# Performance work log

Hardware: AMD Instinct MI355X
Metric: run time of the kernel (lower is better)

## Reference

```python
import jax, jax.numpy as jnp
import numpy as np

BIAS = 1.0
SIGMA = 0.5
EPS = 1e-5


def mrf_loss(gen, target):
    # gen, target: [B, C, H, W]
    mean_t = jnp.mean(target, axis=1, keepdims=True)
    gf = gen - mean_t
    tf = target - mean_t
    gn = gf / jnp.linalg.norm(gf, axis=1, keepdims=True)
    tn = tf / jnp.linalg.norm(tf, axis=1, keepdims=True)
    B, C, H, W = target.shape
    # 1x1 patches of target, ordered by spatial position (matches unfold h,w order)
    patches = tn.transpose(0, 2, 3, 1).reshape(B, H * W, C)  # [B, P, C]
    # per-sample conv2d with 1x1 kernels == batched GEMM
    sim = jnp.einsum('bpc,bchw->bphw', patches, gn)  # [B, P, H, W]
    cosine_dist = -(sim - 1.0) / 2.0
    relative = cosine_dist / (jnp.min(cosine_dist, axis=1, keepdims=True) + EPS)
    dist = jnp.exp((BIAS - relative) / SIGMA)
    cs = dist / jnp.sum(dist, axis=1, keepdims=True)
    k_max = jnp.max(cs.reshape(B, H * W, -1), axis=2)  # [B, P]
    div_mrf = jnp.mean(k_max, axis=1)  # [B]
    return jnp.sum(-jnp.log(div_mrf))


def setup_inputs() -> dict:
    key = jax.random.key(0)
    k1, k2, k3, k4 = jax.random.split(key, 4)
    return {
        'gen_relu3_2': jax.random.normal(k1, (4, 256, 64, 64), dtype=jnp.float32),
        'tar_relu3_2': jax.random.normal(k2, (4, 256, 64, 64), dtype=jnp.float32),
        'gen_relu4_2': jax.random.normal(k3, (4, 512, 32, 32), dtype=jnp.float32),
        'tar_relu4_2': jax.random.normal(k4, (4, 512, 32, 32), dtype=jnp.float32),
    }


def reference(gen_relu3_2, tar_relu3_2, gen_relu4_2, tar_relu4_2):
    # style layers: relu3_2 (w=1.0), relu4_2 (w=1.0); content layers: relu4_2 (w=1.0)
    m3 = mrf_loss(gen_relu3_2, tar_relu3_2)
    m4 = mrf_loss(gen_relu4_2, tar_relu4_2)
    style_loss = (1.0 * m3 + 1.0 * m4) * 1.0  # l_s = 1.0
    content_loss = (1.0 * m4) * 1.0           # l_c = 1.0
    return style_loss + content_loss
```

## Files before the change

### kernel.cpp

```cpp
#include <hip/hip_runtime.h>
#include <math.h>


#define MRF_EPS 1e-5f
#define LOG2E 1.44269504088896340736f

typedef __attribute__((ext_vector_type(8))) short bf16x8;
typedef __attribute__((ext_vector_type(4))) float f32x4;
typedef unsigned short ushort_t;
struct __align__(8) ushort4_t { ushort_t x, y, z, w; };
struct __align__(16) ushort8_t { ushort_t v[8]; };

__device__ __forceinline__ ushort_t f2bf(float x) {
    unsigned u = __float_as_uint(x);
    u += 0x7FFFu + ((u >> 16) & 1u);
    return (ushort_t)(u >> 16);
}
__device__ __forceinline__ float bf2f(ushort_t u) {
    return __uint_as_float(((unsigned)u) << 16);
}

typedef __attribute__((address_space(1))) const unsigned int gu32;
typedef __attribute__((address_space(3))) unsigned int lu32;
__device__ __forceinline__ void gload16(const ushort_t* g, ushort_t* l) {
    __builtin_amdgcn_global_load_lds((gu32*)(uintptr_t)g, (lu32*)(uintptr_t)l,
                                     16, 0, 0);
}

template <int C>
__device__ __forceinline__ void prep_body(
    const float* __restrict__ gen, const float* __restrict__ tar,
    ushort_t* __restrict__ gnT, ushort_t* __restrict__ tnT,
    int S, int b, int bx, char* __restrict__ smem) {
    constexpr int KN = C / 64;
    constexpr int KC = C / 8;
    constexpr int CP = C + 8;
    const int tid = threadIdx.x, pq = tid & 3, cs = tid >> 2;
    const int s0 = bx * 16;

    f32x4* red  = (f32x4*)smem;
    f32x4* red2 = (f32x4*)(smem + 16384);
    ushort_t* tileG = (ushort_t*)smem;
    ushort_t* tileT = tileG + 16 * CP;
    float* sm  = (float*)(smem + 33280);
    float* srt = sm + 16;
    float* srg = sm + 32;

    const float* g = gen + (size_t)b * C * S + s0 + pq * 4;
    const float* t = tar + (size_t)b * C * S + s0 + pq * 4;

    f32x4 gv[KN], tv[KN];
    f32x4 st = {0.f, 0.f, 0.f, 0.f}, st2 = st, sg = st, sg2 = st;
#pragma unroll
    for (int k = 0; k < KN; k++) {
        tv[k] = *(const f32x4*)(t + (size_t)(cs + 64 * k) * S);
        gv[k] = *(const f32x4*)(g + (size_t)(cs + 64 * k) * S);
        st += tv[k]; st2 += tv[k] * tv[k]; sg += gv[k]; sg2 += gv[k] * gv[k];
    }
    red[(0 * 4 + pq) * 64 + cs] = st;  red[(1 * 4 + pq) * 64 + cs] = st2;
    red[(2 * 4 + pq) * 64 + cs] = sg;  red[(3 * 4 + pq) * 64 + cs] = sg2;
    __syncthreads();
    if (tid < 64) {
        int s_ = tid >> 4, p_ = (tid >> 2) & 3, part = tid & 3;
        f32x4 s = red[(s_ * 4 + p_) * 64 + part * 16];
#pragma unroll
        for (int j = 1; j < 16; j++) s += red[(s_ * 4 + p_) * 64 + part * 16 + j];
        red2[(s_ * 4 + p_) * 4 + part] = s;
    }
    __syncthreads();
    if (tid < 4) {
        f32x4 sts  = red2[(0*4+tid)*4+0] + red2[(0*4+tid)*4+1] + red2[(0*4+tid)*4+2] + red2[(0*4+tid)*4+3];
        f32x4 st2s = red2[(1*4+tid)*4+0] + red2[(1*4+tid)*4+1] + red2[(1*4+tid)*4+2] + red2[(1*4+tid)*4+3];
        f32x4 sgs  = red2[(2*4+tid)*4+0] + red2[(2*4+tid)*4+1] + red2[(2*4+tid)*4+2] + red2[(2*4+tid)*4+3];
        f32x4 sg2s = red2[(3*4+tid)*4+0] + red2[(3*4+tid)*4+1] + red2[(3*4+tid)*4+2] + red2[(3*4+tid)*4+3];
        f32x4 m, vrt, vrg;
        float invC = 1.f / (float)C;
#pragma unroll
        for (int e = 0; e < 4; e++) {
            float mm = sts[e] * invC;
            m[e] = mm;
            vrt[e] = rsqrtf(st2s[e] - mm * sts[e]);
            vrg[e] = rsqrtf(sg2s[e] - 2.f * mm * sgs[e] + mm * sts[e]);
        }
        *(f32x4*)&sm[tid * 4] = m;
        *(f32x4*)&srt[tid * 4] = vrt;
        *(f32x4*)&srg[tid * 4] = vrg;
    }
    __syncthreads();
    f32x4 m4  = *(f32x4*)&sm[pq * 4];
    f32x4 rt4 = *(f32x4*)&srt[pq * 4];
    f32x4 rg4 = *(f32x4*)&srg[pq * 4];
#pragma unroll
    for (int k = 0; k < KN; k++) {
        int c = cs + 64 * k;
#pragma unroll
        for (int e = 0; e < 4; e++) {
            tileG[(pq * 4 + e) * CP + c] = f2bf((gv[k][e] - m4[e]) * rg4[e]);
            tileT[(pq * 4 + e) * CP + c] = f2bf((tv[k][e] - m4[e]) * rt4[e]);
        }
    }
    __syncthreads();
    const int lm = tid & 15;
    const int r16 = s0 >> 4;
    size_t obase = (size_t)b * (size_t)S * C;
#pragma unroll
    for (int j = 0; j < KC / 16; j++) {
        int ch = (tid >> 4) + 16 * j;
        size_t off = obase + (((size_t)r16 * KC + ch) * 16 + lm) * 8;
        *(ushort8_t*)(gnT + off) = *(const ushort8_t*)&tileG[lm * CP + ch * 8];
        *(ushort8_t*)(tnT + off) = *(const ushort8_t*)&tileT[lm * CP + ch * 8];
    }
}

__global__ __launch_bounds__(256) void prep_all(
    const float* __restrict__ gen3, const float* __restrict__ tar3,
    const float* __restrict__ gen4, const float* __restrict__ tar4,
    ushort_t* __restrict__ gnT3, ushort_t* __restrict__ tnT3,
    ushort_t* __restrict__ gnT4, ushort_t* __restrict__ tnT4) {
    __shared__ __align__(16) char smem[33536];
    int bid = blockIdx.x;
    if (bid < 256) {
        int z = bid >> 6, bx = bid & 63;
        prep_body<512>(gen4, tar4, gnT4, tnT4, 1024, z, bx, smem);
    } else {
        bid -= 256;
        int z = bid >> 8, bx = bid & 255;
        prep_body<256>(gen3, tar3, gnT3, tnT3, 4096, z, bx, smem);
    }
}

template <int K>
__device__ __forceinline__ void gemm_body(
    const ushort_t* __restrict__ A, const ushort_t* __restrict__ B,
    ushort_t* __restrict__ sim, float* __restrict__ cmPart,
    int S, int bx, int by, ushort_t* __restrict__ lds) {
    const int tid = threadIdx.x;
    const int lane = tid & 63, wave = tid >> 6;
    const int wm = (wave & 1) * 64, wn = (wave >> 1) * 64;
    const int lm = lane & 15, quad = lane >> 4;
    const int q0 = bx * 128;

    constexpr int KC = K / 8;
    constexpr int KB = K / 32;

    const ushort_t* segsrc[4];
    ushort_t* segdst[4];
#pragma unroll
    for (int i = 0; i < 4; i++) {
        int s = wave * 4 + i;
        segsrc[i] = (s < 8)
            ? A + ((size_t)(by * 8 + s) * KC) * 128 + lane * 8
            : B + ((size_t)(bx * 8 + (s - 8)) * KC) * 128 + lane * 8;
        segdst[i] = lds + s * 512;
    }

    auto stage = [&](int buf, int kb) {
#pragma unroll
        for (int i = 0; i < 4; i++)
            gload16(segsrc[i] + (size_t)kb * 512, segdst[i] + buf * 8192);
    };

    f32x4 acc[4][4];
#pragma unroll
    for (int t = 0; t < 4; t++)
#pragma unroll
        for (int u = 0; u < 4; u++) acc[t][u] = (f32x4){0.f, 0.f, 0.f, 0.f};

    stage(0, 0);
    stage(1, 1);
    asm volatile("s_waitcnt vmcnt(4)" ::: "memory");
    __builtin_amdgcn_s_barrier();
    __builtin_amdgcn_sched_barrier(0);

    const ushort_t* lA = lds + (wm >> 4) * 512 + quad * 128 + lm * 8;
    const ushort_t* lB = lds + 4096 + (wn >> 4) * 512 + quad * 128 + lm * 8;

#pragma unroll
    for (int kb = 0; kb < KB; kb++) {
        const int cur = (kb % 3) * 8192;
        if (kb + 2 < KB) stage((kb + 2) % 3, kb + 2);
        bf16x8 a[4], b[4];
#pragma unroll
        for (int t = 0; t < 4; t++) {
            a[t] = *(const bf16x8*)(lA + cur + t * 512);
            b[t] = *(const bf16x8*)(lB + cur + t * 512);
        }
        __builtin_amdgcn_s_setprio(1);
#pragma unroll
        for (int t = 0; t < 4; t++)
#pragma unroll
            for (int u = 0; u < 4; u++)
                acc[t][u] = __builtin_amdgcn_mfma_f32_16x16x32_bf16(a[t], b[u], acc[t][u], 0, 0, 0);
        __builtin_amdgcn_s_setprio(0);
        if (kb + 1 < KB) {
            if (kb + 2 < KB) asm volatile("s_waitcnt vmcnt(4)" ::: "memory");
            else             asm volatile("s_waitcnt vmcnt(0)" ::: "memory");
            __builtin_amdgcn_s_barrier();
            __builtin_amdgcn_sched_barrier(0);
        }
    }

    int nQB = S >> 7;
    size_t base = ((size_t)(by * nQB + bx)) * 16384
                + (size_t)(wave * 4096 + quad * 128 + lm * 8);
    float cmax[4] = {-INFINITY, -INFINITY, -INFINITY, -INFINITY};
#pragma unroll
    for (int t2 = 0; t2 < 2; t2++)
#pragma unroll
        for (int u = 0; u < 4; u++) {
            f32x4 v0 = acc[t2 * 2][u], v1 = acc[t2 * 2 + 1][u];
            ushort8_t o;
            o.v[0] = f2bf(v0.x); o.v[1] = f2bf(v0.y); o.v[2] = f2bf(v0.z); o.v[3] = f2bf(v0.w);
            o.v[4] = f2bf(v1.x); o.v[5] = f2bf(v1.y); o.v[6] = f2bf(v1.z); o.v[7] = f2bf(v1.w);
            *(ushort8_t*)(sim + base + (t2 * 4 + u) * 512) = o;
            float mx = fmaxf(fmaxf(fmaxf(bf2f(o.v[0]), bf2f(o.v[1])), fmaxf(bf2f(o.v[2]), bf2f(o.v[3]))),
                             fmaxf(fmaxf(bf2f(o.v[4]), bf2f(o.v[5])), fmaxf(bf2f(o.v[6]), bf2f(o.v[7]))));
            cmax[u] = fmaxf(cmax[u], mx);
        }
    int r = by * 2 + (wave & 1);
#pragma unroll
    for (int u = 0; u < 4; u++) {
        float m = cmax[u];
        m = fmaxf(m, __shfl_xor(m, 16, 64));
        m = fmaxf(m, __shfl_xor(m, 32, 64));
        if (lane < 16) cmPart[(size_t)r * S + q0 + wn + u * 16 + lane] = m;
    }
}

__global__ __launch_bounds__(256) void gemm_all(
    const ushort_t* __restrict__ tnT3, const ushort_t* __restrict__ gnT3,
    ushort_t* __restrict__ sim3, float* __restrict__ cmPart3,
    const ushort_t* __restrict__ tnT4, const ushort_t* __restrict__ gnT4,
    ushort_t* __restrict__ sim4, float* __restrict__ cmPart4) {
    __shared__ ushort_t lds[24576];
    int bid = blockIdx.x;
    if (bid < 256) {
        int z = bid >> 6, rem = bid & 63, by = rem >> 3, bx = rem & 7;
        gemm_body<512>(tnT4 + (size_t)z * 524288, gnT4 + (size_t)z * 524288,
                       sim4 + (size_t)z * 1048576, cmPart4 + (size_t)z * 16384,
                       1024, bx, by, lds);
    } else {
        bid -= 256;
        int z = bid >> 10, rem = bid & 1023, by = rem >> 5, bx = rem & 31;
        gemm_body<256>(tnT3 + (size_t)z * 1048576, gnT3 + (size_t)z * 1048576,
                       sim3 + (size_t)z * 16777216, cmPart3 + (size_t)z * 262144,
                       4096, bx, by, lds);
    }
}

__global__ __launch_bounds__(256) void colmax_reduce_all(
    const float* __restrict__ cmPart3, float2* __restrict__ coef3, float* __restrict__ colsum3,
    const float* __restrict__ cmPart4, float2* __restrict__ coef4, float* __restrict__ colsum4,
    float* __restrict__ acc) {
    const float* cmPart; float2* coef; float* colsum; int S, R, qb, accIdx;
    int bid = blockIdx.x;
    if (bid < 16) {
        int z = bid >> 2; qb = bid & 3; S = 1024; R = 16; accIdx = 4 + z;
        cmPart = cmPart4 + (size_t)z * 16384; coef = coef4 + (size_t)z * 1024;
        colsum = colsum4 + (size_t)z * 1024;
    } else {
        bid -= 16;
        int z = bid >> 4; qb = bid & 15; S = 4096; R = 64; accIdx = z;
        cmPart = cmPart3 + (size_t)z * 262144; coef = coef3 + (size_t)z * 4096;
        colsum = colsum3 + (size_t)z * 4096;
    }
    if (qb == 0 && threadIdx.x == 0) acc[accIdx] = 0.f;
    int q = qb * 256 + threadIdx.x;
    float m = cmPart[q];
    for (int r = 1; r < R; r++) m = fmaxf(m, cmPart[(size_t)r * S + q]);
    float c1 = 1.f / ((1.f - m) * 0.5f + MRF_EPS);
    coef[q] = make_float2((2.f - c1) * LOG2E, c1 * LOG2E);
    colsum[q] = 0.f;
}

__global__ __launch_bounds__(256) void colsum_all(
    const ushort_t* __restrict__ sim3, const float2* __restrict__ coef3, float* __restrict__ colsum3,
    const ushort_t* __restrict__ sim4, const float2* __restrict__ coef4, float* __restrict__ colsum4) {
    const ushort_t* sim; const float2* coef; float* colsum; int S, bx, by;
    int bid = blockIdx.x;
    if (bid < 256) {
        int z = bid >> 6, rem = bid & 63; by = rem >> 3; bx = rem & 7; S = 1024;
        sim = sim4 + (size_t)z * 1048576; coef = coef4 + (size_t)z * 1024;
        colsum = colsum4 + (size_t)z * 1024;
    } else {
        bid -= 256;
        int z = bid >> 10, rem = bid & 1023; by = rem >> 5; bx = rem & 31; S = 4096;
        sim = sim3 + (size_t)z * 16777216; coef = coef3 + (size_t)z * 4096;
        colsum = colsum3 + (size_t)z * 4096;
    }
    int tid = threadIdx.x, lane = tid & 63;
    int quad = lane >> 4, lm = lane & 15;
    int sub = (tid >> 6) & 1, cg = tid >> 7;
    int slot = sub | (cg << 1);
    int nQB = S >> 7;
    int qb = bx * 128 + cg * 64 + lm;
    float c0[4], c1[4], su[4];
#pragma unroll
    for (int u = 0; u < 4; u++) {
        float2 cc = coef[qb + u * 16];
        c0[u] = cc.x; c1[u] = cc.y; su[u] = 0.f;
    }
    const ushort_t* base = sim + ((size_t)(by * nQB + bx)) * 16384
                         + (size_t)(slot * 4096 + quad * 128 + lm * 8);
#pragma unroll
    for (int t2 = 0; t2 < 2; t2++)
#pragma unroll
        for (int u = 0; u < 4; u++) {
            ushort8_t e = *(const ushort8_t*)(base + (t2 * 4 + u) * 512);
            float s = 0.f;
#pragma unroll
            for (int j = 0; j < 8; j++) s += exp2f(c0[u] + c1[u] * bf2f(e.v[j]));
            su[u] += s;
        }
#pragma unroll
    for (int u = 0; u < 4; u++) {
        su[u] += __shfl_xor(su[u], 16, 64);
        su[u] += __shfl_xor(su[u], 32, 64);
        if (lane < 16) atomicAdd(colsum + qb + u * 16, su[u]);
    }
}

template <int NQB, int NBX>
__device__ __forceinline__ void rowmax_body(
    const ushort_t* __restrict__ sim, const float2* __restrict__ coef,
    const float* __restrict__ colsum, float* __restrict__ rmPart,
    int by, int g) {
    int tid = threadIdx.x, lane = tid & 63, wave = tid >> 6;
    int ph = wave & 1, t2 = wave >> 1;
    int quad = lane >> 4, lm = lane & 15;
    float m[8];
#pragma unroll
    for (int j = 0; j < 8; j++) m[j] = -INFINITY;
    for (int bxi = 0; bxi < NBX; bxi++) {
        int bx = g * NBX + bxi;
        float c0p[8], c1v[8];
#pragma unroll
        for (int cg = 0; cg < 2; cg++)
#pragma unroll
            for (int u = 0; u < 4; u++) {
                int q = bx * 128 + cg * 64 + u * 16 + lm;
                float2 cc = coef[q];
                c0p[cg * 4 + u] = cc.x - log2f(colsum[q]);
                c1v[cg * 4 + u] = cc.y;
            }
        const ushort_t* bb = sim + ((size_t)(by * NQB + bx)) * 16384
                           + (size_t)((t2 * 4) * 512 + quad * 128 + lm * 8);
#pragma unroll
        for (int cg = 0; cg < 2; cg++) {
            int slot = ph + 2 * cg;
#pragma unroll
            for (int u = 0; u < 4; u++) {
                ushort8_t e = *(const ushort8_t*)(bb + slot * 4096 + u * 512);
                float a = c0p[cg * 4 + u], c = c1v[cg * 4 + u];
#pragma unroll
                for (int j = 0; j < 8; j++) m[j] = fmaxf(m[j], a + c * bf2f(e.v[j]));
            }
        }
    }
#pragma unroll
    for (int off = 1; off <= 8; off <<= 1)
#pragma unroll
        for (int j = 0; j < 8; j++) m[j] = fmaxf(m[j], __shfl_xor(m[j], off, 64));
    if (lm == 0) {
        int pbase = by * 128 + ph * 64 + t2 * 32 + quad * 4;
#pragma unroll
        for (int j = 0; j < 8; j++)
            rmPart[pbase + (j >> 2) * 16 + (j & 3)] = m[j];
    }
}

__global__ __launch_bounds__(256) void rowmax_all(
    const ushort_t* __restrict__ sim3, const float2* __restrict__ coef3, const float* __restrict__ colsum3,
    float* __restrict__ rmPart3,
    const ushort_t* __restrict__ sim4, const float2* __restrict__ coef4, const float* __restrict__ colsum4,
    float* __restrict__ rmPart4) {
    int bid = blockIdx.x;
    if (bid < 1024) {
        int z = bid >> 8, rem = bid & 255, by = rem >> 3, g = rem & 7;
        rowmax_body<32, 4>(sim3 + (size_t)z * 16777216, coef3 + (size_t)z * 4096,
                           colsum3 + (size_t)z * 4096,
                           rmPart3 + ((size_t)(z * 8 + g)) * 4096, by, g);
    } else {
        bid -= 1024;
        int z = bid >> 5, rem = bid & 31, by = rem >> 2, g = rem & 3;
        rowmax_body<8, 2>(sim4 + (size_t)z * 1048576, coef4 + (size_t)z * 1024,
                          colsum4 + (size_t)z * 1024,
                          rmPart4 + ((size_t)(z * 4 + g)) * 1024, by, g);
    }
}

__global__ __launch_bounds__(256) void rmreduce_all(
    const float* __restrict__ rmPart3, const float* __restrict__ rmPart4,
    float* __restrict__ acc) {
    const float* rm; int G, stride, p; float* slot;
    int bid = blockIdx.x;
    if (bid < 64) {
        int z = bid >> 4, blk = bid & 15; G = 8; stride = 4096;
        rm = rmPart3 + (size_t)z * 8 * 4096;
        p = blk * 256 + threadIdx.x; slot = acc + z;
    } else {
        bid -= 64;
        int z = bid >> 2, blk = bid & 3; G = 4; stride = 1024;
        rm = rmPart4 + (size_t)z * 4 * 1024;
        p = blk * 256 + threadIdx.x; slot = acc + 4 + z;
    }
    float m = rm[p];
    for (int g = 1; g < G; g++) m = fmaxf(m, rm[(size_t)g * stride + p]);
    float k = exp2f(m);
#pragma unroll
    for (int off = 32; off >= 1; off >>= 1) k += __shfl_xor(k, off, 64);
    __shared__ float part[4];
    if ((threadIdx.x & 63) == 0) part[threadIdx.x >> 6] = k;
    __syncthreads();
    if (threadIdx.x == 0)
        atomicAdd(slot, part[0] + part[1] + part[2] + part[3]);
}

__global__ void finalize_kernel(const float* __restrict__ acc, float* __restrict__ out) {
    float loss = 0.f;
    for (int b = 0; b < 4; b++) loss += -logf(acc[b] * (1.f / 4096.f));
    for (int b = 0; b < 4; b++) loss += -2.f * logf(acc[4 + b] * (1.f / 1024.f));
    out[0] = loss;
}

extern "C" void kernel_launch(void* const* d_in, const int* in_sizes, int n_in,
                              void* d_out, int out_size, void* d_ws, size_t ws_size,
                              hipStream_t stream) {
    const float* gen3 = (const float*)d_in[0];
    const float* tar3 = (const float*)d_in[1];
    const float* gen4 = (const float*)d_in[2];
    const float* tar4 = (const float*)d_in[3];

    char* wsb = (char*)d_ws;
    size_t off = 0;
    auto alloc = [&](size_t bytes) {
        void* p = wsb + off;
        off += (bytes + 255) & ~(size_t)255;
        return p;
    };
    ushort_t* sim3 = (ushort_t*)alloc((size_t)4 * 16777216 * 2);
    ushort_t* gnT3 = (ushort_t*)alloc((size_t)4 * 1048576 * 2);
    ushort_t* tnT3 = (ushort_t*)alloc((size_t)4 * 1048576 * 2);
    float* cmPart3 = (float*)alloc((size_t)4 * 262144 * 4);
    float2* coef3 = (float2*)alloc((size_t)4 * 4096 * 8);
    float* colsum3 = (float*)alloc((size_t)4 * 4096 * 4);
    float* rmPart3 = (float*)alloc((size_t)4 * 8 * 4096 * 4);
    ushort_t* sim4 = (ushort_t*)alloc((size_t)4 * 1048576 * 2);
    ushort_t* gnT4 = (ushort_t*)alloc((size_t)4 * 524288 * 2);
    ushort_t* tnT4 = (ushort_t*)alloc((size_t)4 * 524288 * 2);
    float* cmPart4 = (float*)alloc((size_t)4 * 16384 * 4);
    float2* coef4 = (float2*)alloc((size_t)4 * 1024 * 8);
    float* colsum4 = (float*)alloc((size_t)4 * 1024 * 4);
    float* rmPart4 = (float*)alloc((size_t)4 * 4 * 1024 * 4);
    float* acc = (float*)alloc(64 * 4);

    prep_all<<<256 + 1024, 256, 0, stream>>>(
        gen3, tar3, gen4, tar4, gnT3, tnT3, gnT4, tnT4);
    gemm_all<<<256 + 4096, 256, 0, stream>>>(
        tnT3, gnT3, sim3, cmPart3, tnT4, gnT4, sim4, cmPart4);
    colmax_reduce_all<<<16 + 64, 256, 0, stream>>>(
        cmPart3, coef3, colsum3, cmPart4, coef4, colsum4, acc);
    colsum_all<<<256 + 4096, 256, 0, stream>>>(
        sim3, coef3, colsum3, sim4, coef4, colsum4);
    rowmax_all<<<1024 + 128, 256, 0, stream>>>(
        sim3, coef3, colsum3, rmPart3, sim4, coef4, colsum4, rmPart4);
    rmreduce_all<<<64 + 16, 256, 0, stream>>>(rmPart3, rmPart4, acc);
    finalize_kernel<<<1, 1, 0, stream>>>(acc, (float*)d_out);
}
```

Before: 216.0 us.

## Fuse row-max reduction via atomicMax, batch colsum tiles, use nontemporal sim stores

```diff
diff --git a/kernel.cpp b/kernel.cpp
--- a/kernel.cpp
+++ b/kernel.cpp
@@ -7,7 +7,9 @@
 
 typedef __attribute__((ext_vector_type(8))) short bf16x8;
 typedef __attribute__((ext_vector_type(4))) float f32x4;
+typedef __attribute__((ext_vector_type(4))) unsigned int uint32x4;
 typedef unsigned short ushort_t;
+typedef unsigned int uint_t;
 struct __align__(8) ushort4_t { ushort_t x, y, z, w; };
 struct __align__(16) ushort8_t { ushort_t v[8]; };
 
@@ -18,6 +20,13 @@
 }
 __device__ __forceinline__ float bf2f(ushort_t u) {
     return __uint_as_float(((unsigned)u) << 16);
+}
+__device__ __forceinline__ uint_t encf(float f) {
+    uint_t b = __float_as_uint(f);
+    return (b & 0x80000000u) ? ~b : (b | 0x80000000u);
+}
+__device__ __forceinline__ float decf(uint_t u) {
+    return __uint_as_float((u & 0x80000000u) ? (u ^ 0x80000000u) : ~u);
 }
 
 typedef __attribute__((address_space(1))) const unsigned int gu32;
@@ -212,7 +221,8 @@
             ushort8_t o;
             o.v[0] = f2bf(v0.x); o.v[1] = f2bf(v0.y); o.v[2] = f2bf(v0.z); o.v[3] = f2bf(v0.w);
             o.v[4] = f2bf(v1.x); o.v[5] = f2bf(v1.y); o.v[6] = f2bf(v1.z); o.v[7] = f2bf(v1.w);
-            *(ushort8_t*)(sim + base + (t2 * 4 + u) * 512) = o;
+            __builtin_nontemporal_store(*(const uint32x4*)&o,
+                                        (uint32x4*)(sim + base + (t2 * 4 + u) * 512));
             float mx = fmaxf(fmaxf(fmaxf(bf2f(o.v[0]), bf2f(o.v[1])), fmaxf(bf2f(o.v[2]), bf2f(o.v[3]))),
                              fmaxf(fmaxf(bf2f(o.v[4]), bf2f(o.v[5])), fmaxf(bf2f(o.v[6]), bf2f(o.v[7]))));
             cmax[u] = fmaxf(cmax[u], mx);
@@ -251,20 +261,21 @@
 __global__ __launch_bounds__(256) void colmax_reduce_all(
     const float* __restrict__ cmPart3, float2* __restrict__ coef3, float* __restrict__ colsum3,
     const float* __restrict__ cmPart4, float2* __restrict__ coef4, float* __restrict__ colsum4,
-    float* __restrict__ acc) {
-    const float* cmPart; float2* coef; float* colsum; int S, R, qb, accIdx;
+    uint_t* __restrict__ rmMax3, uint_t* __restrict__ rmMax4) {
+    const float* cmPart; float2* coef; float* colsum; int S, R, qb;
     int bid = blockIdx.x;
     if (bid < 16) {
-        int z = bid >> 2; qb = bid & 3; S = 1024; R = 16; accIdx = 4 + z;
+        int z = bid >> 2; qb = bid & 3; S = 1024; R = 16;
         cmPart = cmPart4 + (size_t)z * 16384; coef = coef4 + (size_t)z * 1024;
         colsum = colsum4 + (size_t)z * 1024;
+        rmMax4[bid * 256 + threadIdx.x] = 0u;
     } else {
         bid -= 16;
-        int z = bid >> 4; qb = bid & 15; S = 4096; R = 64; accIdx = z;
+        int z = bid >> 4; qb = bid & 15; S = 4096; R = 64;
         cmPart = cmPart3 + (size_t)z * 262144; coef = coef3 + (size_t)z * 4096;
         colsum = colsum3 + (size_t)z * 4096;
-    }
-    if (qb == 0 && threadIdx.x == 0) acc[accIdx] = 0.f;
+        rmMax3[bid * 256 + threadIdx.x] = 0u;
+    }
     int q = qb * 256 + threadIdx.x;
     float m = cmPart[q];
     for (int r = 1; r < R; r++) m = fmaxf(m, cmPart[(size_t)r * S + q]);
@@ -276,15 +287,15 @@
 __global__ __launch_bounds__(256) void colsum_all(
     const ushort_t* __restrict__ sim3, const float2* __restrict__ coef3, float* __restrict__ colsum3,
     const ushort_t* __restrict__ sim4, const float2* __restrict__ coef4, float* __restrict__ colsum4) {
-    const ushort_t* sim; const float2* coef; float* colsum; int S, bx, by;
+    const ushort_t* sim; const float2* coef; float* colsum; int S, bx, by0;
     int bid = blockIdx.x;
-    if (bid < 256) {
-        int z = bid >> 6, rem = bid & 63; by = rem >> 3; bx = rem & 7; S = 1024;
+    if (bid < 64) {
+        int z = bid >> 4, rem = bid & 15; bx = rem >> 1; by0 = (rem & 1) * 4; S = 1024;
         sim = sim4 + (size_t)z * 1048576; coef = coef4 + (size_t)z * 1024;
         colsum = colsum4 + (size_t)z * 1024;
     } else {
-        bid -= 256;
-        int z = bid >> 10, rem = bid & 1023; by = rem >> 5; bx = rem & 31; S = 4096;
+        bid -= 64;
+        int z = bid >> 8, rem = bid & 255; bx = rem >> 3; by0 = (rem & 7) * 4; S = 4096;
         sim = sim3 + (size_t)z * 16777216; coef = coef3 + (size_t)z * 4096;
         colsum = colsum3 + (size_t)z * 4096;
     }
@@ -300,18 +311,21 @@
         float2 cc = coef[qb + u * 16];
         c0[u] = cc.x; c1[u] = cc.y; su[u] = 0.f;
     }
-    const ushort_t* base = sim + ((size_t)(by * nQB + bx)) * 16384
-                         + (size_t)(slot * 4096 + quad * 128 + lm * 8);
-#pragma unroll
-    for (int t2 = 0; t2 < 2; t2++)
-#pragma unroll
-        for (int u = 0; u < 4; u++) {
-            ushort8_t e = *(const ushort8_t*)(base + (t2 * 4 + u) * 512);
-            float s = 0.f;
-#pragma unroll
-            for (int j = 0; j < 8; j++) s += exp2f(c0[u] + c1[u] * bf2f(e.v[j]));
-            su[u] += s;
-        }
+#pragma unroll
+    for (int byi = 0; byi < 4; byi++) {
+        const ushort_t* base = sim + ((size_t)((by0 + byi) * nQB + bx)) * 16384
+                             + (size_t)(slot * 4096 + quad * 128 + lm * 8);
+#pragma unroll
+        for (int t2 = 0; t2 < 2; t2++)
+#pragma unroll
+            for (int u = 0; u < 4; u++) {
+                ushort8_t e = *(const ushort8_t*)(base + (t2 * 4 + u) * 512);
+                float s = 0.f;
+#pragma unroll
+                for (int j = 0; j < 8; j++) s += exp2f(c0[u] + c1[u] * bf2f(e.v[j]));
+                su[u] += s;
+            }
+    }
 #pragma unroll
     for (int u = 0; u < 4; u++) {
         su[u] += __shfl_xor(su[u], 16, 64);
@@ -323,7 +337,7 @@
 template <int NQB, int NBX>
 __device__ __forceinline__ void rowmax_body(
     const ushort_t* __restrict__ sim, const float2* __restrict__ coef,
-    const float* __restrict__ colsum, float* __restrict__ rmPart,
+    const float* __restrict__ colsum, uint_t* __restrict__ rmMax,
     int by, int g) {
     int tid = threadIdx.x, lane = tid & 63, wave = tid >> 6;
     int ph = wave & 1, t2 = wave >> 1;
@@ -365,62 +379,58 @@
         int pbase = by * 128 + ph * 64 + t2 * 32 + quad * 4;
 #pragma unroll
         for (int j = 0; j < 8; j++)
-            rmPart[pbase + (j >> 2) * 16 + (j & 3)] = m[j];
+            atomicMax(rmMax + pbase + (j >> 2) * 16 + (j & 3), encf(m[j]));
     }
 }
 
 __global__ __launch_bounds__(256) void rowmax_all(
     const ushort_t* __restrict__ sim3, const float2* __restrict__ coef3, const float* __restrict__ colsum3,
-    float* __restrict__ rmPart3,
+    uint_t* __restrict__ rmMax3,
     const ushort_t* __restrict__ sim4, const float2* __restrict__ coef4, const float* __restrict__ colsum4,
-    float* __restrict__ rmPart4) {
+    uint_t* __restrict__ rmMax4) {
     int bid = blockIdx.x;
     if (bid < 1024) {
         int z = bid >> 8, rem = bid & 255, by = rem >> 3, g = rem & 7;
         rowmax_body<32, 4>(sim3 + (size_t)z * 16777216, coef3 + (size_t)z * 4096,
                            colsum3 + (size_t)z * 4096,
-                           rmPart3 + ((size_t)(z * 8 + g)) * 4096, by, g);
+                           rmMax3 + (size_t)z * 4096, by, g);
     } else {
         bid -= 1024;
         int z = bid >> 5, rem = bid & 31, by = rem >> 2, g = rem & 3;
         rowmax_body<8, 2>(sim4 + (size_t)z * 1048576, coef4 + (size_t)z * 1024,
                           colsum4 + (size_t)z * 1024,
-                          rmPart4 + ((size_t)(z * 4 + g)) * 1024, by, g);
-    }
-}
-
-__global__ __launch_bounds__(256) void rmreduce_all(
-    const float* __restrict__ rmPart3, const float* __restrict__ rmPart4,
-    float* __restrict__ acc) {
-    const float* rm; int G, stride, p; float* slot;
-    int bid = blockIdx.x;
-    if (bid < 64) {
-        int z = bid >> 4, blk = bid & 15; G = 8; stride = 4096;
-        rm = rmPart3 + (size_t)z * 8 * 4096;
-        p = blk * 256 + threadIdx.x; slot = acc + z;
-    } else {
-        bid -= 64;
-        int z = bid >> 2, blk = bid & 3; G = 4; stride = 1024;
-        rm = rmPart4 + (size_t)z * 4 * 1024;
-        p = blk * 256 + threadIdx.x; slot = acc + 4 + z;
-    }
-    float m = rm[p];
-    for (int g = 1; g < G; g++) m = fmaxf(m, rm[(size_t)g * stride + p]);
-    float k = exp2f(m);
-#pragma unroll
-    for (int off = 32; off >= 1; off >>= 1) k += __shfl_xor(k, off, 64);
-    __shared__ float part[4];
-    if ((threadIdx.x & 63) == 0) part[threadIdx.x >> 6] = k;
+                          rmMax4 + (size_t)z * 1024, by, g);
+    }
+}
+
+__global__ __launch_bounds__(256) void finalize_kernel(
+    const uint_t* __restrict__ rmMax3, const uint_t* __restrict__ rmMax4,
+    float* __restrict__ out) {
+    int tid = threadIdx.x, lane = tid & 63, wave = tid >> 6;
+    float s[8] = {0.f, 0.f, 0.f, 0.f, 0.f, 0.f, 0.f, 0.f};
+    for (int i = tid; i < 16384; i += 256) s[i >> 12] += exp2f(decf(rmMax3[i]));
+    for (int i = tid; i < 4096; i += 256) s[4 + (i >> 10)] += exp2f(decf(rmMax4[i]));
+#pragma unroll
+    for (int k = 0; k < 8; k++)
+#pragma unroll
+        for (int off = 32; off >= 1; off >>= 1) s[k] += __shfl_xor(s[k], off, 64);
+    __shared__ float red[8][4];
+    if (lane == 0)
+#pragma unroll
+        for (int k = 0; k < 8; k++) red[k][wave] = s[k];
     __syncthreads();
-    if (threadIdx.x == 0)
-        atomicAdd(slot, part[0] + part[1] + part[2] + part[3]);
-}
-
-__global__ void finalize_kernel(const float* __restrict__ acc, float* __restrict__ out) {
-    float loss = 0.f;
-    for (int b = 0; b < 4; b++) loss += -logf(acc[b] * (1.f / 4096.f));
-    for (int b = 0; b < 4; b++) loss += -2.f * logf(acc[4 + b] * (1.f / 1024.f));
-    out[0] = loss;
+    if (tid == 0) {
+        float loss = 0.f;
+        for (int b = 0; b < 4; b++) {
+            float v3 = red[b][0] + red[b][1] + red[b][2] + red[b][3];
+            loss += -logf(v3 * (1.f / 4096.f));
+        }
+        for (int b = 0; b < 4; b++) {
+            float v4 = red[4 + b][0] + red[4 + b][1] + red[4 + b][2] + red[4 + b][3];
+            loss += -2.f * logf(v4 * (1.f / 1024.f));
+        }
+        out[0] = loss;
+    }
 }
 
 extern "C" void kernel_launch(void* const* d_in, const int* in_sizes, int n_in,
@@ -444,26 +454,24 @@
     float* cmPart3 = (float*)alloc((size_t)4 * 262144 * 4);
     float2* coef3 = (float2*)alloc((size_t)4 * 4096 * 8);
     float* colsum3 = (float*)alloc((size_t)4 * 4096 * 4);
-    float* rmPart3 = (float*)alloc((size_t)4 * 8 * 4096 * 4);
+    uint_t* rmMax3 = (uint_t*)alloc((size_t)4 * 4096 * 4);
     ushort_t* sim4 = (ushort_t*)alloc((size_t)4 * 1048576 * 2);
     ushort_t* gnT4 = (ushort_t*)alloc((size_t)4 * 524288 * 2);
     ushort_t* tnT4 = (ushort_t*)alloc((size_t)4 * 524288 * 2);
     float* cmPart4 = (float*)alloc((size_t)4 * 16384 * 4);
     float2* coef4 = (float2*)alloc((size_t)4 * 1024 * 8);
     float* colsum4 = (float*)alloc((size_t)4 * 1024 * 4);
-    float* rmPart4 = (float*)alloc((size_t)4 * 4 * 1024 * 4);
-    float* acc = (float*)alloc(64 * 4);
+    uint_t* rmMax4 = (uint_t*)alloc((size_t)4 * 1024 * 4);
 
     prep_all<<<256 + 1024, 256, 0, stream>>>(
         gen3, tar3, gen4, tar4, gnT3, tnT3, gnT4, tnT4);
     gemm_all<<<256 + 4096, 256, 0, stream>>>(
         tnT3, gnT3, sim3, cmPart3, tnT4, gnT4, sim4, cmPart4);
     colmax_reduce_all<<<16 + 64, 256, 0, stream>>>(
-        cmPart3, coef3, colsum3, cmPart4, coef4, colsum4, acc);
-    colsum_all<<<256 + 4096, 256, 0, stream>>>(
+        cmPart3, coef3, colsum3, cmPart4, coef4, colsum4, rmMax3, rmMax4);
+    colsum_all<<<64 + 1024, 256, 0, stream>>>(
         sim3, coef3, colsum3, sim4, coef4, colsum4);
     rowmax_all<<<1024 + 128, 256, 0, stream>>>(
-        sim3, coef3, colsum3, rmPart3, sim4, coef4, colsum4, rmPart4);
-    rmreduce_all<<<64 + 16, 256, 0, stream>>>(rmPart3, rmPart4, acc);
-    finalize_kernel<<<1, 1, 0, stream>>>(acc, (float*)d_out);
-}
+        sim3, coef3, colsum3, rmMax3, sim4, coef4, colsum4, rmMax4);
+    finalize_kernel<<<1, 256, 0, stream>>>(rmMax3, rmMax4, (float*)d_out);
+}
```

Result: slower. 254.0 us (+17.6%).
